# Optimization experiments

Hardware: AMD Instinct MI355X
Metric: run time of the kernel (lower is better)

Reference implementation:

```python
import jax, jax.numpy as jnp
import numpy as np

D, L, W_DIM, K = 16, 16, 16, 6
N = D * L * W_DIM
STD_POSITION = 1.0
STD_INTENSITY = 3.0


def _dist_weight():
    # pairwise Gaussian of squared Euclidean distance between voxel coords
    gx, gy, gz = jnp.meshgrid(jnp.arange(D, dtype=jnp.float32),
                              jnp.arange(L, dtype=jnp.float32),
                              jnp.arange(W_DIM, dtype=jnp.float32),
                              indexing='ij')
    sq = jnp.zeros((N, N), dtype=jnp.float32)
    for g in (gx, gy, gz):  # fixed 3-axis loop, accumulate per-axis [N,N] diffs
        v = g.reshape(-1)
        sq = sq + jnp.square(v[:, None] - v[None, :])
    return jnp.exp(-sq / (STD_POSITION ** 2))


def setup_inputs() -> dict:
    key = jax.random.key(0)
    k1, k2 = jax.random.split(key)
    patch = jax.random.uniform(k1, (D, L, W_DIM), dtype=jnp.float32)
    prob = jax.random.uniform(k2, (D, L, W_DIM, K), dtype=jnp.float32)
    return {"patch": patch, "prob": prob, "dist_weight": _dist_weight(), "k": K}


def reference(patch, prob, dist_weight, k):
    f = patch.reshape(-1)  # [N]
    # intensity affinity: exp(-((fi - fj)/std_intensity)^2), detached in original
    intensity = jnp.exp(-jnp.square((f[:, None] - f[None, :]) / STD_INTENSITY))
    weights = jax.lax.stop_gradient(intensity) * dist_weight  # [N, N]
    P = prob.reshape(-1, k)  # [N, K], matches prob[:,:,:,t].reshape(-1)
    WP = weights @ P                       # [N, K]
    num = jnp.sum(P * WP, axis=0)          # sum_ij w_ij p_i p_j per class
    den = P.T @ jnp.sum(weights, axis=1)   # sum_ij w_ij p_i per class
    loss = jnp.float32(k) - jnp.sum(num / den)
    return loss.astype(jnp.float32)
```

## Files before the change

kernel.cpp:

```cpp
#include <hip/hip_runtime.h>

#define KK 6
#define RAD 3
#define NOFF 7
#define NGRP 49
#define NBLK (16 * NGRP)
#define C_INT (-0.16029944898766259f)
#define C_POS (-1.4426950408889634f)
#define MAGIC 0x7F3D9B21u

__global__ void __launch_bounds__(256) sncut_fused(
    const float* __restrict__ patch,
    const float* __restrict__ prob,
    float* __restrict__ out,
    unsigned* __restrict__ flags,
    float* __restrict__ bpart)
{
    const int slice = blockIdx.x / NGRP;
    const int og    = blockIdx.x % NGRP;
    const int dx    = og / NOFF - RAD;
    const int dy    = og % NOFF - RAD;

    const int t = threadIdx.x;
    const int i = (slice << 8) + t;
    const int y = t >> 4, z = t & 15;

    const int xj = slice + dx;
    const int yj = y + dy;
    const bool vxy = ((unsigned)xj < 16u) & ((unsigned)yj < 16u);
    const int jbase = (xj << 8) + (yj << 4);

    const float fi = patch[i];
    const float2* __restrict__ P2 = reinterpret_cast<const float2*>(prob);
    const float2 pi0 = P2[i * 3], pi1 = P2[i * 3 + 1], pi2 = P2[i * 3 + 2];

    const float sqxy = C_POS * (float)(dx * dx + dy * dy);

    float s0 = 0.f, s1 = 0.f, s2 = 0.f, s3 = 0.f, s4 = 0.f, s5 = 0.f, r = 0.f;

    #pragma unroll
    for (int dz = -RAD; dz <= RAD; ++dz) {
        const int zj = z + dz;
        const bool valid = vxy & ((unsigned)zj < 16u);
        const int jj = valid ? (jbase + zj) : i;
        const float fj = patch[jj];
        const float2 q0 = P2[jj * 3], q1 = P2[jj * 3 + 1], q2 = P2[jj * 3 + 2];
        const float df = fi - fj;
        const float sqc = sqxy + (float)(dz * dz) * C_POS;
        float w = exp2f(fmaf(df * df, C_INT, sqc));
        w = valid ? w : 0.f;
        r += w;
        s0 = fmaf(w, q0.x, s0); s1 = fmaf(w, q0.y, s1);
        s2 = fmaf(w, q1.x, s2); s3 = fmaf(w, q1.y, s3);
        s4 = fmaf(w, q2.x, s4); s5 = fmaf(w, q2.y, s5);
    }

    float v[12];
    v[0] = s0 * pi0.x; v[1] = s1 * pi0.y; v[2] = s2 * pi1.x;
    v[3] = s3 * pi1.y; v[4] = s4 * pi2.x; v[5] = s5 * pi2.y;
    v[6] = r * pi0.x;  v[7] = r * pi0.y;  v[8] = r * pi1.x;
    v[9] = r * pi1.y;  v[10] = r * pi2.x; v[11] = r * pi2.y;

    #pragma unroll
    for (int m = 32; m >= 1; m >>= 1) {
        #pragma unroll
        for (int c = 0; c < 12; ++c) v[c] += __shfl_xor(v[c], m);
    }

    __shared__ float ls[4][12];
    const int wave = t >> 6, lane = t & 63;
    if (lane == 0) {
        #pragma unroll
        for (int c = 0; c < 12; ++c) ls[wave][c] = v[c];
    }
    __syncthreads();
    if (t < 12) {
        const float p = ls[0][t] + ls[1][t] + ls[2][t] + ls[3][t];
        __hip_atomic_store(&bpart[blockIdx.x * 12 + t], p,
                           __ATOMIC_RELAXED, __HIP_MEMORY_SCOPE_AGENT);
    }
    if (t == 0) {
        asm volatile("s_waitcnt vmcnt(0)" ::: "memory");
        __hip_atomic_store(&flags[blockIdx.x], MAGIC,
                           __ATOMIC_RELAXED, __HIP_MEMORY_SCOPE_AGENT);
    }

    if (blockIdx.x != NBLK - 1) return;

    for (;;) {
        int ok = 1;
        for (int b = t; b < NBLK; b += 256)
            ok &= (__hip_atomic_load(&flags[b], __ATOMIC_RELAXED,
                                     __HIP_MEMORY_SCOPE_AGENT) == MAGIC);
        if (__syncthreads_and(ok)) break;
        __builtin_amdgcn_s_sleep(2);
    }
    (void)__hip_atomic_load(&flags[0], __ATOMIC_ACQUIRE, __HIP_MEMORY_SCOPE_AGENT);

    for (int b = t; b < NBLK; b += 256)
        __hip_atomic_store(&flags[b], 0u, __ATOMIC_RELAXED, __HIP_MEMORY_SCOPE_AGENT);

    float a[12];
    #pragma unroll
    for (int c = 0; c < 12; ++c) a[c] = 0.f;

    for (int row = t; row < NBLK; row += 256) {
        const float4* rp = reinterpret_cast<const float4*>(bpart + row * 12);
        const float4 b0 = rp[0], b1 = rp[1], b2 = rp[2];
        a[0] += b0.x; a[1] += b0.y; a[2]  += b0.z; a[3]  += b0.w;
        a[4] += b1.x; a[5] += b1.y; a[6]  += b1.z; a[7]  += b1.w;
        a[8] += b2.x; a[9] += b2.y; a[10] += b2.z; a[11] += b2.w;
    }

    #pragma unroll
    for (int m = 32; m >= 1; m >>= 1) {
        #pragma unroll
        for (int c = 0; c < 12; ++c) a[c] += __shfl_xor(a[c], m);
    }

    __syncthreads();
    if (lane == 0) {
        #pragma unroll
        for (int c = 0; c < 12; ++c) ls[wave][c] = a[c];
    }
    __syncthreads();
    if (t == 0) {
        float loss = (float)KK;
        #pragma unroll
        for (int c = 0; c < KK; ++c) {
            const float num = ls[0][c]     + ls[1][c]     + ls[2][c]     + ls[3][c];
            const float den = ls[0][c + 6] + ls[1][c + 6] + ls[2][c + 6] + ls[3][c + 6];
            loss -= num / den;
        }
        out[0] = loss;
    }
}

extern "C" void kernel_launch(void* const* d_in, const int* in_sizes, int n_in,
                              void* d_out, int out_size, void* d_ws, size_t ws_size,
                              hipStream_t stream) {
    const float* patch = (const float*)d_in[0];
    const float* prob  = (const float*)d_in[1];
    float* out = (float*)d_out;
    unsigned* flags = (unsigned*)d_ws;
    float* bpart    = (float*)((char*)d_ws + 4096);

    sncut_fused<<<NBLK, 256, 0, stream>>>(patch, prob, out, flags, bpart);
}
```

Before: 14.67 us.

## Replace single last-block reduction with two-level hierarchical cross-block reduction

Previously only the final block waited on flags from all 784 blocks and then summed all partials. Now the 49 blocks of the last slice each wait on and sum the partials of their 16-block column, and publish a group partial with a second flag. Block 48 then gathers the 48 group partials and computes the loss. The goal is to spread the final reduction and flag polling across many blocks so the serial tail is shorter. The cost is more spin-waiting blocks and extra workspace flags.

After: 14.92 us. No clear change (+1.7%).

```diff
diff --git a/kernel.cpp b/kernel.cpp
--- a/kernel.cpp
+++ b/kernel.cpp
@@ -14,6 +14,8 @@
     const float* __restrict__ prob,
     float* __restrict__ out,
     unsigned* __restrict__ flags,
+    unsigned* __restrict__ gflags,
+    float* __restrict__ gpart,
     float* __restrict__ bpart)
 {
     const int slice = blockIdx.x / NGRP;
@@ -85,53 +87,85 @@
                            __ATOMIC_RELAXED, __HIP_MEMORY_SCOPE_AGENT);
     }
 
-    if (blockIdx.x != NBLK - 1) return;
+    if (slice != 15) return;
+
+    __shared__ float gl[16][13];
+    __shared__ float g48[12];
+    __shared__ float sums[12];
 
     for (;;) {
         int ok = 1;
-        for (int b = t; b < NBLK; b += 256)
-            ok &= (__hip_atomic_load(&flags[b], __ATOMIC_RELAXED,
-                                     __HIP_MEMORY_SCOPE_AGENT) == MAGIC);
+        if (t < 16)
+            ok = (__hip_atomic_load(&flags[t * NGRP + og], __ATOMIC_RELAXED,
+                                    __HIP_MEMORY_SCOPE_AGENT) == MAGIC);
         if (__syncthreads_and(ok)) break;
-        __builtin_amdgcn_s_sleep(2);
+        __builtin_amdgcn_s_sleep(1);
     }
-    (void)__hip_atomic_load(&flags[0], __ATOMIC_ACQUIRE, __HIP_MEMORY_SCOPE_AGENT);
+    if (t < 192) {
+        const int s = t / 12, c = t % 12;
+        gl[s][c] = __hip_atomic_load(&bpart[(s * NGRP + og) * 12 + c],
+                                     __ATOMIC_RELAXED, __HIP_MEMORY_SCOPE_AGENT);
+    }
+    if (t < 16)
+        __hip_atomic_store(&flags[t * NGRP + og], 0u,
+                           __ATOMIC_RELAXED, __HIP_MEMORY_SCOPE_AGENT);
+    __syncthreads();
 
-    for (int b = t; b < NBLK; b += 256)
-        __hip_atomic_store(&flags[b], 0u, __ATOMIC_RELAXED, __HIP_MEMORY_SCOPE_AGENT);
-
-    float a[12];
-    #pragma unroll
-    for (int c = 0; c < 12; ++c) a[c] = 0.f;
-
-    for (int row = t; row < NBLK; row += 256) {
-        const float4* rp = reinterpret_cast<const float4*>(bpart + row * 12);
-        const float4 b0 = rp[0], b1 = rp[1], b2 = rp[2];
-        a[0] += b0.x; a[1] += b0.y; a[2]  += b0.z; a[3]  += b0.w;
-        a[4] += b1.x; a[5] += b1.y; a[6]  += b1.z; a[7]  += b1.w;
-        a[8] += b2.x; a[9] += b2.y; a[10] += b2.z; a[11] += b2.w;
+    float g = 0.f;
+    if (t < 12) {
+        #pragma unroll
+        for (int s = 0; s < 16; ++s) g += gl[s][t];
     }
 
-    #pragma unroll
-    for (int m = 32; m >= 1; m >>= 1) {
-        #pragma unroll
-        for (int c = 0; c < 12; ++c) a[c] += __shfl_xor(a[c], m);
+    if (og != 48) {
+        if (t < 12)
+            __hip_atomic_store(&gpart[og * 12 + t], g,
+                               __ATOMIC_RELAXED, __HIP_MEMORY_SCOPE_AGENT);
+        if (t == 0) {
+            asm volatile("s_waitcnt vmcnt(0)" ::: "memory");
+            __hip_atomic_store(&gflags[og], MAGIC,
+                               __ATOMIC_RELAXED, __HIP_MEMORY_SCOPE_AGENT);
+        }
+        return;
     }
 
+    if (t < 12) g48[t] = g;
     __syncthreads();
-    if (lane == 0) {
+
+    for (;;) {
+        int ok = 1;
+        if (t < 48)
+            ok = (__hip_atomic_load(&gflags[t], __ATOMIC_RELAXED,
+                                    __HIP_MEMORY_SCOPE_AGENT) == MAGIC);
+        if (__syncthreads_and(ok)) break;
+        __builtin_amdgcn_s_sleep(1);
+    }
+    if (t < 192) {
+        const int part = t / 12, c = t % 12;
+        float acc = 0.f;
         #pragma unroll
-        for (int c = 0; c < 12; ++c) ls[wave][c] = a[c];
+        for (int q = 0; q < 3; ++q)
+            acc += __hip_atomic_load(&gpart[(part * 3 + q) * 12 + c],
+                                     __ATOMIC_RELAXED, __HIP_MEMORY_SCOPE_AGENT);
+        gl[part][c] = acc;
+    }
+    if (t < 48)
+        __hip_atomic_store(&gflags[t], 0u,
+                           __ATOMIC_RELAXED, __HIP_MEMORY_SCOPE_AGENT);
+    __syncthreads();
+
+    if (t < 12) {
+        float tot = 0.f;
+        #pragma unroll
+        for (int part = 0; part < 16; ++part) tot += gl[part][t];
+        sums[t] = tot + g48[t];
     }
     __syncthreads();
     if (t == 0) {
         float loss = (float)KK;
         #pragma unroll
-        for (int c = 0; c < KK; ++c) {
-            const float num = ls[0][c]     + ls[1][c]     + ls[2][c]     + ls[3][c];
-            const float den = ls[0][c + 6] + ls[1][c + 6] + ls[2][c + 6] + ls[3][c + 6];
-            loss -= num / den;
-        }
+        for (int c = 0; c < KK; ++c)
+            loss -= sums[c] / sums[c + 6];
         out[0] = loss;
     }
 }
@@ -142,8 +176,10 @@
     const float* patch = (const float*)d_in[0];
     const float* prob  = (const float*)d_in[1];
     float* out = (float*)d_out;
-    unsigned* flags = (unsigned*)d_ws;
-    float* bpart    = (float*)((char*)d_ws + 4096);
+    unsigned* flags  = (unsigned*)d_ws;
+    unsigned* gflags = (unsigned*)((char*)d_ws + 3584);
+    float*    gpart  = (float*)((char*)d_ws + 4096);
+    float*    bpart  = (float*)((char*)d_ws + 8192);
 
-    sncut_fused<<<NBLK, 256, 0, stream>>>(patch, prob, out, flags, bpart);
+    sncut_fused<<<NBLK, 256, 0, stream>>>(patch, prob, out, flags, gflags, gpart, bpart);
 }
```

## Add dedicated reducer block that consumes partials in chunks as they complete

Applied to the files above, without the earlier changes.

Instead of making the last compute block wait for every other block and then reduce all partials, an extra block is launched that waits for each 196-block chunk of flags and reduces that chunk while later blocks are still computing. This is meant to overlap the final reduction with the tail of the main computation and shorten the serialized epilogue. It adds a spinning block that takes up a CU slot. If that block is scheduled early it spins while other blocks work, and there is no acquire fence after the flag wait, so ordering rests on relaxed atomic loads.

After: 25.91 us. 76.6% more time.

```diff
diff --git a/kernel.cpp b/kernel.cpp
--- a/kernel.cpp
+++ b/kernel.cpp
@@ -5,6 +5,8 @@
 #define NOFF 7
 #define NGRP 49
 #define NBLK (16 * NGRP)
+#define CSZ 196
+#define NCH 4
 #define C_INT (-0.16029944898766259f)
 #define C_POS (-1.4426950408889634f)
 #define MAGIC 0x7F3D9B21u
@@ -16,12 +18,65 @@
     unsigned* __restrict__ flags,
     float* __restrict__ bpart)
 {
+    const int t = threadIdx.x;
+
+    if (blockIdx.x == NBLK) {
+        __shared__ float gl[CSZ][13];
+        __shared__ float gl2[16][12];
+        __shared__ float sums[12];
+        float run = 0.f;
+
+        for (int q = 0; q < NCH; ++q) {
+            const int base = q * CSZ;
+            for (;;) {
+                int ok = 1;
+                if (t < CSZ)
+                    ok = (__hip_atomic_load(&flags[base + t], __ATOMIC_RELAXED,
+                                            __HIP_MEMORY_SCOPE_AGENT) == MAGIC);
+                if (__syncthreads_and(ok)) break;
+                __builtin_amdgcn_s_sleep(1);
+            }
+            for (int u = t; u < CSZ * 12; u += 256) {
+                const int row = u / 12, c = u - row * 12;
+                gl[row][c] = __hip_atomic_load(&bpart[(base + row) * 12 + c],
+                                               __ATOMIC_RELAXED,
+                                               __HIP_MEMORY_SCOPE_AGENT);
+            }
+            if (t < CSZ)
+                __hip_atomic_store(&flags[base + t], 0u,
+                                   __ATOMIC_RELAXED, __HIP_MEMORY_SCOPE_AGENT);
+            __syncthreads();
+            if (t < 192) {
+                const int s = t / 12, c = t - (t / 12) * 12;
+                float a = 0.f;
+                for (int row = s; row < CSZ; row += 16) a += gl[row][c];
+                gl2[s][c] = a;
+            }
+            __syncthreads();
+            if (t < 12) {
+                float a = 0.f;
+                #pragma unroll
+                for (int s = 0; s < 16; ++s) a += gl2[s][t];
+                run += a;
+            }
+            __syncthreads();
+        }
+        if (t < 12) sums[t] = run;
+        __syncthreads();
+        if (t == 0) {
+            float loss = (float)KK;
+            #pragma unroll
+            for (int c = 0; c < KK; ++c) loss -= sums[c] / sums[c + 6];
+            out[0] = loss;
+        }
+        return;
+    }
+
     const int slice = blockIdx.x / NGRP;
     const int og    = blockIdx.x % NGRP;
     const int dx    = og / NOFF - RAD;
     const int dy    = og % NOFF - RAD;
 
-    const int t = threadIdx.x;
     const int i = (slice << 8) + t;
     const int y = t >> 4, z = t & 15;
 
@@ -84,56 +139,6 @@
         __hip_atomic_store(&flags[blockIdx.x], MAGIC,
                            __ATOMIC_RELAXED, __HIP_MEMORY_SCOPE_AGENT);
     }
-
-    if (blockIdx.x != NBLK - 1) return;
-
-    for (;;) {
-        int ok = 1;
-        for (int b = t; b < NBLK; b += 256)
-            ok &= (__hip_atomic_load(&flags[b], __ATOMIC_RELAXED,
-                                     __HIP_MEMORY_SCOPE_AGENT) == MAGIC);
-        if (__syncthreads_and(ok)) break;
-        __builtin_amdgcn_s_sleep(2);
-    }
-    (void)__hip_atomic_load(&flags[0], __ATOMIC_ACQUIRE, __HIP_MEMORY_SCOPE_AGENT);
-
-    for (int b = t; b < NBLK; b += 256)
-        __hip_atomic_store(&flags[b], 0u, __ATOMIC_RELAXED, __HIP_MEMORY_SCOPE_AGENT);
-
-    float a[12];
-    #pragma unroll
-    for (int c = 0; c < 12; ++c) a[c] = 0.f;
-
-    for (int row = t; row < NBLK; row += 256) {
-        const float4* rp = reinterpret_cast<const float4*>(bpart + row * 12);
-        const float4 b0 = rp[0], b1 = rp[1], b2 = rp[2];
-        a[0] += b0.x; a[1] += b0.y; a[2]  += b0.z; a[3]  += b0.w;
-        a[4] += b1.x; a[5] += b1.y; a[6]  += b1.z; a[7]  += b1.w;
-        a[8] += b2.x; a[9] += b2.y; a[10] += b2.z; a[11] += b2.w;
-    }
-
-    #pragma unroll
-    for (int m = 32; m >= 1; m >>= 1) {
-        #pragma unroll
-        for (int c = 0; c < 12; ++c) a[c] += __shfl_xor(a[c], m);
-    }
-
-    __syncthreads();
-    if (lane == 0) {
-        #pragma unroll
-        for (int c = 0; c < 12; ++c) ls[wave][c] = a[c];
-    }
-    __syncthreads();
-    if (t == 0) {
-        float loss = (float)KK;
-        #pragma unroll
-        for (int c = 0; c < KK; ++c) {
-            const float num = ls[0][c]     + ls[1][c]     + ls[2][c]     + ls[3][c];
-            const float den = ls[0][c + 6] + ls[1][c + 6] + ls[2][c + 6] + ls[3][c + 6];
-            loss -= num / den;
-        }
-        out[0] = loss;
-    }
 }
 
 extern "C" void kernel_launch(void* const* d_in, const int* in_sizes, int n_in,
@@ -145,5 +150,5 @@
     unsigned* flags = (unsigned*)d_ws;
     float* bpart    = (float*)((char*)d_ws + 4096);
 
-    sncut_fused<<<NBLK, 256, 0, stream>>>(patch, prob, out, flags, bpart);
+    sncut_fused<<<NBLK + 1, 256, 0, stream>>>(patch, prob, out, flags, bpart);
 }
```
